# Kernel tuning notes

Measured on AMD Instinct MI355X. Metric: run time of the kernel, lower is better.

## Reference

```python
import jax, jax.numpy as jnp
import numpy as np

IN_DIM = 256
K = 64
NB = 64  # num_blocks
N = NB * K
BATCH = 4096
DT = 0.05
TAU_EPS = 1e-6


def setup_inputs() -> dict:
    key = jax.random.key(0)
    ks = jax.random.split(key, 10)
    def xavier(k_, shape, fan_in, fan_out):
        lim = np.sqrt(6.0 / (fan_in + fan_out))
        return jax.random.uniform(k_, shape, jnp.float32, -lim, lim)
    return {
        "y": jax.random.normal(ks[0], (BATCH, N), jnp.float32),
        "u_t": jax.random.normal(ks[1], (BATCH, IN_DIM), jnp.float32),
        "tau_raw": jnp.zeros((N,), jnp.float32),
        "W_in_w": xavier(ks[2], (K, IN_DIM), IN_DIM, K),
        "W_in_b": jnp.zeros((K,), jnp.float32),
        "W_fwd_w": xavier(ks[3], (NB - 1, K, K), K, K),
        "W_fwd_b": jnp.zeros((NB - 1, K), jnp.float32),
        "W_rec_w": xavier(ks[4], (NB, K, K), K, K),
        "W_rec_b": jnp.zeros((NB, K), jnp.float32),
        "E_l": xavier(ks[5], (NB, K, K), K, K),
        "E_l_r": xavier(ks[6], (NB, K, K), K, K),
    }


def reference(y, u_t, tau_raw, W_in_w, W_in_b, W_fwd_w, W_fwd_b, W_rec_w, W_rec_b, E_l, E_l_r):
    yb = y.reshape(-1, NB, K)  # [batch, B, k]
    tau = jax.nn.softplus(tau_raw).reshape(NB, K) + TAU_EPS  # [B, k]
    # input drive for block 0 (torch Linear: x @ W^T + b)
    net0 = jnp.tanh(u_t @ W_in_w.T + W_in_b)  # [batch, k]
    # forward coupling for blocks 1..B-1, batched over blocks
    prev = yb[:, :-1, :]  # [batch, B-1, k]
    net_fwd = jnp.tanh(jnp.einsum('bji,joi->bjo', prev, W_fwd_w) + W_fwd_b)
    net_out = jnp.concatenate([net0[:, None, :], net_fwd], axis=1)  # [batch, B, k]
    # recurrent coupling, all blocks
    net_rec = jnp.tanh(jnp.einsum('bji,joi->bjo', yb, W_rec_w) + W_rec_b)
    decay = 1.0 / tau + jnp.abs(net_out) + jnp.abs(net_rec)  # [batch, B, k]
    drive = jnp.einsum('joi,bji->bjo', E_l, net_out) + jnp.einsum('joi,bji->bjo', E_l_r, net_rec)
    y_new = (yb + DT * drive) / (1.0 + DT * decay)
    return y_new.reshape(-1, N)
```

## Files before the change

### kernel.cpp

```cpp
#include <hip/hip_runtime.h>


#define IN_DIM 256
#define K 64
#define NB 64
#define BATCH 4096
#define NTOT (NB * K)
#define DTC 0.05f
#define TAU_EPS 1e-6f
#define LDSTR 72

typedef __bf16 bf16;
typedef bf16 bf16x8 __attribute__((ext_vector_type(8)));
typedef bf16 bf16x4 __attribute__((ext_vector_type(4)));
typedef float f32x4 __attribute__((ext_vector_type(4)));

__device__ __forceinline__ float fast_tanh(float x) {
    float e = __expf(2.0f * x);
    return 1.0f - 2.0f * __builtin_amdgcn_rcpf(e + 1.0f);
}

__device__ __forceinline__ void stage64(bf16* __restrict__ dst,
                                        const float* __restrict__ src,
                                        int gstride, int tid) {
#pragma unroll
    for (int it = 0; it < 2; ++it) {
        int idx = it * 512 + tid;
        int r = idx >> 4;
        int c4 = idx & 15;
        float4 v = *(const float4*)(src + r * gstride + (c4 << 2));
        bf16x4 p = { (bf16)v.x, (bf16)v.y, (bf16)v.z, (bf16)v.w };
        *(bf16x4*)(dst + r * LDSTR + (c4 << 2)) = p;
    }
}

__device__ __forceinline__ void load_afrag(const float* __restrict__ rowp,
                                           bf16x8& f0, bf16x8& f1) {
    float4 a0 = *(const float4*)(rowp);
    float4 a1 = *(const float4*)(rowp + 4);
    float4 a2 = *(const float4*)(rowp + 32);
    float4 a3 = *(const float4*)(rowp + 36);
    f0 = (bf16x8){ (bf16)a0.x, (bf16)a0.y, (bf16)a0.z, (bf16)a0.w,
                   (bf16)a1.x, (bf16)a1.y, (bf16)a1.z, (bf16)a1.w };
    f1 = (bf16x8){ (bf16)a2.x, (bf16)a2.y, (bf16)a2.z, (bf16)a2.w,
                   (bf16)a3.x, (bf16)a3.y, (bf16)a3.z, (bf16)a3.w };
}

__global__ __launch_bounds__(512, 4)
void ltcn_kernel(const float* __restrict__ y, const float* __restrict__ u_t,
                 const float* __restrict__ tau_raw,
                 const float* __restrict__ W_in_w, const float* __restrict__ W_in_b,
                 const float* __restrict__ W_fwd_w, const float* __restrict__ W_fwd_b,
                 const float* __restrict__ W_rec_w, const float* __restrict__ W_rec_b,
                 const float* __restrict__ E_l, const float* __restrict__ E_l_r,
                 float* __restrict__ out) {
    __shared__ bf16 sWf [64 * LDSTR];
    __shared__ bf16 sWr [64 * LDSTR];
    __shared__ bf16 sEl [64 * LDSTR];
    __shared__ bf16 sElr[64 * LDSTR];
    __shared__ bf16 sNo [128 * LDSTR];
    __shared__ bf16 sNr [128 * LDSTR];
    __shared__ float sInvTau[64], sBf[64], sBr[64];

    const int tid  = threadIdx.x;
    const int j    = blockIdx.y;
    const int b0   = blockIdx.x * 128;
    const int wave = tid >> 6;
    const int lane = tid & 63;
    const int quad = lane >> 4;
    const int l16  = lane & 15;
    const int am   = wave * 16 + l16;

    stage64(sWr,  W_rec_w + (size_t)j * K * K, K, tid);
    stage64(sEl,  E_l     + (size_t)j * K * K, K, tid);
    stage64(sElr, E_l_r   + (size_t)j * K * K, K, tid);

    bf16x8 yc0, yc1;
    load_afrag(y + (size_t)(b0 + am) * NTOT + j * K + quad * 8, yc0, yc1);

    bf16x8 yp0, yp1;
    if (j != 0) {
        stage64(sWf, W_fwd_w + (size_t)(j - 1) * K * K, K, tid);
        load_afrag(y + (size_t)(b0 + am) * NTOT + (j - 1) * K + quad * 8, yp0, yp1);
    } else {
        stage64(sWf,              W_in_w,       IN_DIM, tid);
        stage64(sNo,              W_in_w + 64,  IN_DIM, tid);
        stage64(sNo + 64 * LDSTR, W_in_w + 128, IN_DIM, tid);
        stage64(sNr,              W_in_w + 192, IN_DIM, tid);
        load_afrag(u_t + (size_t)(b0 + am) * IN_DIM + quad * 8, yp0, yp1);
    }
    if (tid < 64) {
        float x = tau_raw[j * K + tid];
        float sp = (x > 15.0f) ? x : log1pf(__expf(x));
        sInvTau[tid] = 1.0f / (sp + TAU_EPS);
        sBf[tid] = (j == 0) ? W_in_b[tid] : W_fwd_b[(j - 1) * K + tid];
        sBr[tid] = W_rec_b[j * K + tid];
    }
    __syncthreads();

    f32x4 accF[4] = {}, accR[4] = {};
    const int boff = quad * 8;
#pragma unroll
    for (int ct = 0; ct < 4; ++ct) {
        const bf16* br = sWr + (ct * 16 + l16) * LDSTR + boff;
        accR[ct] = __builtin_amdgcn_mfma_f32_16x16x32_bf16(yc0, *(const bf16x8*)br,        accR[ct], 0, 0, 0);
        accR[ct] = __builtin_amdgcn_mfma_f32_16x16x32_bf16(yc1, *(const bf16x8*)(br + 32), accR[ct], 0, 0, 0);
    }
    if (j != 0) {
#pragma unroll
        for (int ct = 0; ct < 4; ++ct) {
            const bf16* bw = sWf + (ct * 16 + l16) * LDSTR + boff;
            accF[ct] = __builtin_amdgcn_mfma_f32_16x16x32_bf16(yp0, *(const bf16x8*)bw,        accF[ct], 0, 0, 0);
            accF[ct] = __builtin_amdgcn_mfma_f32_16x16x32_bf16(yp1, *(const bf16x8*)(bw + 32), accF[ct], 0, 0, 0);
        }
    } else {
        const bf16* chunkB[4] = { sWf, sNo, sNo + 64 * LDSTR, sNr };
#pragma unroll
        for (int kc = 0; kc < 4; ++kc) {
            if (kc)
                load_afrag(u_t + (size_t)(b0 + am) * IN_DIM + kc * 64 + quad * 8, yp0, yp1);
#pragma unroll
            for (int ct = 0; ct < 4; ++ct) {
                const bf16* bw = chunkB[kc] + (ct * 16 + l16) * LDSTR + boff;
                accF[ct] = __builtin_amdgcn_mfma_f32_16x16x32_bf16(yp0, *(const bf16x8*)bw,        accF[ct], 0, 0, 0);
                accF[ct] = __builtin_amdgcn_mfma_f32_16x16x32_bf16(yp1, *(const bf16x8*)(bw + 32), accF[ct], 0, 0, 0);
            }
        }
    }

    float ye[4][4];
    const float* yep = y + (size_t)(b0 + wave * 16 + quad * 4) * NTOT + (size_t)j * K + l16;
#pragma unroll
    for (int ct = 0; ct < 4; ++ct)
#pragma unroll
        for (int r = 0; r < 4; ++r)
            ye[ct][r] = yep[(size_t)r * NTOT + ct * 16];

    float absum[4][4];
#pragma unroll
    for (int ct = 0; ct < 4; ++ct) {
        float bfv = sBf[ct * 16 + l16];
        float brv = sBr[ct * 16 + l16];
#pragma unroll
        for (int r = 0; r < 4; ++r) {
            float no = fast_tanh(accF[ct][r] + bfv);
            float nr = fast_tanh(accR[ct][r] + brv);
            accF[ct][r] = no;
            accR[ct][r] = nr;
            absum[ct][r] = fabsf(no) + fabsf(nr);
        }
    }

    if (j == 0) __syncthreads();

#pragma unroll
    for (int ct = 0; ct < 4; ++ct) {
#pragma unroll
        for (int r = 0; r < 4; ++r) {
            int m = wave * 16 + quad * 4 + r;
            int n = ct * 16 + l16;
            sNo[m * LDSTR + n] = (bf16)accF[ct][r];
            sNr[m * LDSTR + n] = (bf16)accR[ct][r];
        }
    }

    const bf16* aOp = sNo + am * LDSTR + boff;
    const bf16* aRp = sNr + am * LDSTR + boff;
    bf16x8 aO0 = *(const bf16x8*)aOp, aO1 = *(const bf16x8*)(aOp + 32);
    bf16x8 aR0 = *(const bf16x8*)aRp, aR1 = *(const bf16x8*)(aRp + 32);

    f32x4 accD[4] = {};
#pragma unroll
    for (int ct = 0; ct < 4; ++ct) {
        const bf16* bo = sEl  + (ct * 16 + l16) * LDSTR + boff;
        const bf16* br = sElr + (ct * 16 + l16) * LDSTR + boff;
        accD[ct] = __builtin_amdgcn_mfma_f32_16x16x32_bf16(aO0, *(const bf16x8*)bo,        accD[ct], 0, 0, 0);
        accD[ct] = __builtin_amdgcn_mfma_f32_16x16x32_bf16(aO1, *(const bf16x8*)(bo + 32), accD[ct], 0, 0, 0);
        accD[ct] = __builtin_amdgcn_mfma_f32_16x16x32_bf16(aR0, *(const bf16x8*)br,        accD[ct], 0, 0, 0);
        accD[ct] = __builtin_amdgcn_mfma_f32_16x16x32_bf16(aR1, *(const bf16x8*)(br + 32), accD[ct], 0, 0, 0);
    }

    float it4[4];
#pragma unroll
    for (int ct = 0; ct < 4; ++ct) it4[ct] = sInvTau[ct * 16 + l16];

#pragma unroll
    for (int ct = 0; ct < 4; ++ct) {
#pragma unroll
        for (int r = 0; r < 4; ++r) {
            size_t gi = (size_t)(b0 + wave * 16 + quad * 4 + r) * NTOT + j * K + ct * 16 + l16;
            float decay = it4[ct] + absum[ct][r];
            out[gi] = (ye[ct][r] + DTC * accD[ct][r]) * __builtin_amdgcn_rcpf(1.0f + DTC * decay);
        }
    }
}

extern "C" void kernel_launch(void* const* d_in, const int* in_sizes, int n_in,
                              void* d_out, int out_size, void* d_ws, size_t ws_size,
                              hipStream_t stream) {
    const float* y       = (const float*)d_in[0];
    const float* u_t     = (const float*)d_in[1];
    const float* tau_raw = (const float*)d_in[2];
    const float* W_in_w  = (const float*)d_in[3];
    const float* W_in_b  = (const float*)d_in[4];
    const float* W_fwd_w = (const float*)d_in[5];
    const float* W_fwd_b = (const float*)d_in[6];
    const float* W_rec_w = (const float*)d_in[7];
    const float* W_rec_b = (const float*)d_in[8];
    const float* E_l     = (const float*)d_in[9];
    const float* E_l_r   = (const float*)d_in[10];
    float* out = (float*)d_out;

    dim3 grid(BATCH / 128, NB);
    hipLaunchKernelGGL(ltcn_kernel, grid, dim3(512), 0, stream,
                       y, u_t, tau_raw, W_in_w, W_in_b, W_fwd_w, W_fwd_b,
                       W_rec_w, W_rec_b, E_l, E_l_r, out);
}
```

Baseline: 160.6 us.

## Shrink LDS footprint by reusing weight buffers for activations and raise occupancy

Removes the dedicated sNo/sNr shared arrays (about 36KB) and has each wave reuse a 16-row band of the already consumed sWf/sWr buffers as a scratch area for the tanh activations, processed one after the other. For block 0 the input projection now streams W_in_w through sWf in four chunks with barriers. The y epilogue load is moved later and launch_bounds raised to 8 blocks per SM to shrink LDS and register use and fit more waves. The cost is extra barriers and serialized stores and reloads, plus tighter register limits that may cause spills.

```diff
diff --git a/kernel.cpp b/kernel.cpp
--- a/kernel.cpp
+++ b/kernel.cpp
@@ -46,7 +46,7 @@
                    (bf16)a3.x, (bf16)a3.y, (bf16)a3.z, (bf16)a3.w };
 }
 
-__global__ __launch_bounds__(512, 4)
+__global__ __launch_bounds__(512, 8)
 void ltcn_kernel(const float* __restrict__ y, const float* __restrict__ u_t,
                  const float* __restrict__ tau_raw,
                  const float* __restrict__ W_in_w, const float* __restrict__ W_in_b,
@@ -58,8 +58,6 @@
     __shared__ bf16 sWr [64 * LDSTR];
     __shared__ bf16 sEl [64 * LDSTR];
     __shared__ bf16 sElr[64 * LDSTR];
-    __shared__ bf16 sNo [128 * LDSTR];
-    __shared__ bf16 sNr [128 * LDSTR];
     __shared__ float sInvTau[64], sBf[64], sBr[64];
 
     const int tid  = threadIdx.x;
@@ -83,10 +81,7 @@
         stage64(sWf, W_fwd_w + (size_t)(j - 1) * K * K, K, tid);
         load_afrag(y + (size_t)(b0 + am) * NTOT + (j - 1) * K + quad * 8, yp0, yp1);
     } else {
-        stage64(sWf,              W_in_w,       IN_DIM, tid);
-        stage64(sNo,              W_in_w + 64,  IN_DIM, tid);
-        stage64(sNo + 64 * LDSTR, W_in_w + 128, IN_DIM, tid);
-        stage64(sNr,              W_in_w + 192, IN_DIM, tid);
+        stage64(sWf, W_in_w, IN_DIM, tid);
         load_afrag(u_t + (size_t)(b0 + am) * IN_DIM + quad * 8, yp0, yp1);
     }
     if (tid < 64) {
@@ -114,83 +109,90 @@
             accF[ct] = __builtin_amdgcn_mfma_f32_16x16x32_bf16(yp1, *(const bf16x8*)(bw + 32), accF[ct], 0, 0, 0);
         }
     } else {
-        const bf16* chunkB[4] = { sWf, sNo, sNo + 64 * LDSTR, sNr };
-#pragma unroll
+#pragma unroll 1
         for (int kc = 0; kc < 4; ++kc) {
-            if (kc)
-                load_afrag(u_t + (size_t)(b0 + am) * IN_DIM + kc * 64 + quad * 8, yp0, yp1);
 #pragma unroll
             for (int ct = 0; ct < 4; ++ct) {
-                const bf16* bw = chunkB[kc] + (ct * 16 + l16) * LDSTR + boff;
+                const bf16* bw = sWf + (ct * 16 + l16) * LDSTR + boff;
                 accF[ct] = __builtin_amdgcn_mfma_f32_16x16x32_bf16(yp0, *(const bf16x8*)bw,        accF[ct], 0, 0, 0);
                 accF[ct] = __builtin_amdgcn_mfma_f32_16x16x32_bf16(yp1, *(const bf16x8*)(bw + 32), accF[ct], 0, 0, 0);
             }
-        }
-    }
-
-    float ye[4][4];
-    const float* yep = y + (size_t)(b0 + wave * 16 + quad * 4) * NTOT + (size_t)j * K + l16;
-#pragma unroll
-    for (int ct = 0; ct < 4; ++ct)
-#pragma unroll
-        for (int r = 0; r < 4; ++r)
-            ye[ct][r] = yep[(size_t)r * NTOT + ct * 16];
+            if (kc < 3) {
+                load_afrag(u_t + (size_t)(b0 + am) * IN_DIM + (kc + 1) * 64 + quad * 8, yp0, yp1);
+                __syncthreads();
+                stage64(sWf, W_in_w + (kc + 1) * 64, IN_DIM, tid);
+                __syncthreads();
+            }
+        }
+    }
 
     float absum[4][4];
 #pragma unroll
     for (int ct = 0; ct < 4; ++ct) {
         float bfv = sBf[ct * 16 + l16];
         float brv = sBr[ct * 16 + l16];
+        float itv = sInvTau[ct * 16 + l16];
 #pragma unroll
         for (int r = 0; r < 4; ++r) {
             float no = fast_tanh(accF[ct][r] + bfv);
             float nr = fast_tanh(accR[ct][r] + brv);
             accF[ct][r] = no;
             accR[ct][r] = nr;
-            absum[ct][r] = fabsf(no) + fabsf(nr);
-        }
-    }
-
-    if (j == 0) __syncthreads();
-
-#pragma unroll
-    for (int ct = 0; ct < 4; ++ct) {
-#pragma unroll
-        for (int r = 0; r < 4; ++r) {
-            int m = wave * 16 + quad * 4 + r;
-            int n = ct * 16 + l16;
-            sNo[m * LDSTR + n] = (bf16)accF[ct][r];
-            sNr[m * LDSTR + n] = (bf16)accR[ct][r];
-        }
-    }
-
-    const bf16* aOp = sNo + am * LDSTR + boff;
-    const bf16* aRp = sNr + am * LDSTR + boff;
-    bf16x8 aO0 = *(const bf16x8*)aOp, aO1 = *(const bf16x8*)(aOp + 32);
-    bf16x8 aR0 = *(const bf16x8*)aRp, aR1 = *(const bf16x8*)(aRp + 32);
+            absum[ct][r] = itv + fabsf(no) + fabsf(nr);
+        }
+    }
+    __syncthreads();
+
+    bf16* band = (wave < 4) ? (sWf + wave * 16 * LDSTR)
+                            : (sWr + (wave - 4) * 16 * LDSTR);
+    const bf16* ap = band + l16 * LDSTR + boff;
+
+#pragma unroll
+    for (int ct = 0; ct < 4; ++ct)
+#pragma unroll
+        for (int r = 0; r < 4; ++r)
+            band[(quad * 4 + r) * LDSTR + ct * 16 + l16] = (bf16)accF[ct][r];
+
+    bf16x8 aO0 = *(const bf16x8*)ap, aO1 = *(const bf16x8*)(ap + 32);
 
     f32x4 accD[4] = {};
 #pragma unroll
     for (int ct = 0; ct < 4; ++ct) {
-        const bf16* bo = sEl  + (ct * 16 + l16) * LDSTR + boff;
-        const bf16* br = sElr + (ct * 16 + l16) * LDSTR + boff;
+        const bf16* bo = sEl + (ct * 16 + l16) * LDSTR + boff;
         accD[ct] = __builtin_amdgcn_mfma_f32_16x16x32_bf16(aO0, *(const bf16x8*)bo,        accD[ct], 0, 0, 0);
         accD[ct] = __builtin_amdgcn_mfma_f32_16x16x32_bf16(aO1, *(const bf16x8*)(bo + 32), accD[ct], 0, 0, 0);
+    }
+
+#pragma unroll
+    for (int ct = 0; ct < 4; ++ct)
+#pragma unroll
+        for (int r = 0; r < 4; ++r)
+            band[(quad * 4 + r) * LDSTR + ct * 16 + l16] = (bf16)accR[ct][r];
+
+    bf16x8 aR0 = *(const bf16x8*)ap, aR1 = *(const bf16x8*)(ap + 32);
+
+    float ye[4][4];
+    const float* yep = y + (size_t)(b0 + wave * 16 + quad * 4) * NTOT + (size_t)j * K + l16;
+#pragma unroll
+    for (int ct = 0; ct < 4; ++ct)
+#pragma unroll
+        for (int r = 0; r < 4; ++r)
+            ye[ct][r] = yep[(size_t)r * NTOT + ct * 16];
+
+#pragma unroll
+    for (int ct = 0; ct < 4; ++ct) {
+        const bf16* br = sElr + (ct * 16 + l16) * LDSTR + boff;
         accD[ct] = __builtin_amdgcn_mfma_f32_16x16x32_bf16(aR0, *(const bf16x8*)br,        accD[ct], 0, 0, 0);
         accD[ct] = __builtin_amdgcn_mfma_f32_16x16x32_bf16(aR1, *(const bf16x8*)(br + 32), accD[ct], 0, 0, 0);
     }
 
-    float it4[4];
-#pragma unroll
-    for (int ct = 0; ct < 4; ++ct) it4[ct] = sInvTau[ct * 16 + l16];
-
 #pragma unroll
     for (int ct = 0; ct < 4; ++ct) {
 #pragma unroll
         for (int r = 0; r < 4; ++r) {
             size_t gi = (size_t)(b0 + wave * 16 + quad * 4 + r) * NTOT + j * K + ct * 16 + l16;
-            float decay = it4[ct] + absum[ct][r];
-            out[gi] = (ye[ct][r] + DTC * accD[ct][r]) * __builtin_amdgcn_rcpf(1.0f + DTC * decay);
+            out[gi] = (ye[ct][r] + DTC * accD[ct][r])
+                      * __builtin_amdgcn_rcpf(1.0f + DTC * absum[ct][r]);
         }
     }
 }
```

Measured after the change: 183.3 us. +14.2%, slower.
